# Performance work log

Hardware: AMD Instinct MI355X
Metric: run time of the kernel (lower is better)

The kernel has to match this reference:

```python
import jax, jax.numpy as jnp
import numpy as np

N_NODES = 200000
N_EDGES = 600000
N_GRAPHS = 10000
F_NODE = 32
F_EDGE = 16
H = 128
BN_EPS = 1e-5


def setup_inputs() -> dict:
    key = jax.random.key(0)
    ks = jax.random.split(key, 16)

    def rn(k, shape, scale=0.05):
        return jax.random.normal(k, shape, jnp.float32) * scale

    inp = {}
    inp['x'] = jax.random.normal(ks[0], (N_NODES, F_NODE), jnp.float32)
    inp['edge_index'] = jax.random.randint(ks[1], (2, N_EDGES), 0, N_NODES)
    inp['edge_attr'] = jax.random.normal(ks[2], (N_EDGES, F_EDGE), jnp.float32)
    inp['batch'] = jnp.sort(jax.random.randint(ks[3], (N_NODES,), 0, N_GRAPHS))
    # GIN MLP params for 3 conv layers: Linear(din,H) -> BN(H) -> ReLU -> Linear(H,H)
    dims = [F_NODE, H, H]
    i = 4
    for l, din in enumerate(dims, 1):
        inp[f'w1_{l}'] = rn(ks[i], (din, H)); i += 1
        inp[f'b1_{l}'] = jnp.zeros((H,), jnp.float32)
        inp[f'gamma_{l}'] = jnp.ones((H,), jnp.float32)
        inp[f'beta_{l}'] = jnp.zeros((H,), jnp.float32)
        inp[f'rmean_{l}'] = jnp.zeros((H,), jnp.float32)  # BN running stats (eval mode)
        inp[f'rvar_{l}'] = jnp.ones((H,), jnp.float32)
        inp[f'w2_{l}'] = rn(ks[i], (H, H)); i += 1
        inp[f'b2_{l}'] = jnp.zeros((H,), jnp.float32)
    inp['w_e'] = rn(ks[i], (F_EDGE, H)); i += 1
    inp['b_e'] = jnp.zeros((H,), jnp.float32)
    inp['w_fc1'] = rn(ks[i], (H, H // 2)); i += 1
    inp['b_fc1'] = jnp.zeros((H // 2,), jnp.float32)
    inp['w_fc2'] = rn(ks[i], (H // 2, 1)); i += 1
    inp['b_fc2'] = jnp.zeros((1,), jnp.float32)
    return inp


def _gin_conv(x, edge_index, w1, b1, gamma, beta, rmean, rvar, w2, b2):
    # GINConv with eps=0: mlp((1+eps)*x + sum_{j in N(i)} x_j)
    src, dst = edge_index[0], edge_index[1]
    agg = jax.ops.segment_sum(x[src], dst, num_segments=N_NODES)  # scatter-add
    h = x + agg
    h = h @ w1 + b1
    h = (h - rmean) * jax.lax.rsqrt(rvar + BN_EPS) * gamma + beta  # BN eval mode
    h = jax.nn.relu(h)
    return h @ w2 + b2


def reference(x, edge_index, edge_attr, batch,
              w1_1, b1_1, gamma_1, beta_1, rmean_1, rvar_1, w2_1, b2_1,
              w1_2, b1_2, gamma_2, beta_2, rmean_2, rvar_2, w2_2, b2_2,
              w1_3, b1_3, gamma_3, beta_3, rmean_3, rvar_3, w2_3, b2_3,
              w_e, b_e, w_fc1, b_fc1, w_fc2, b_fc2):
    # edge embedding is computed in the original forward but never used
    _edge_emb = edge_attr @ w_e + b_e
    h = jax.nn.relu(_gin_conv(x, edge_index, w1_1, b1_1, gamma_1, beta_1, rmean_1, rvar_1, w2_1, b2_1))
    h = jax.nn.relu(_gin_conv(h, edge_index, w1_2, b1_2, gamma_2, beta_2, rmean_2, rvar_2, w2_2, b2_2))
    h = jax.nn.relu(_gin_conv(h, edge_index, w1_3, b1_3, gamma_3, beta_3, rmean_3, rvar_3, w2_3, b2_3))
    pooled = jax.ops.segment_sum(h, batch, num_segments=N_GRAPHS)  # global_add_pool
    h = jax.nn.relu(pooled @ w_fc1 + b_fc1)
    # dropout: identity in eval mode
    return h @ w_fc2 + b_fc2  # [N_GRAPHS, 1]
```

## Files before the change

kernel.cpp:

```cpp
#include <hip/hip_runtime.h>

#define N_NODES 200000
#define N_EDGES 600000
#define N_GRAPHS 10000
#define F_NODE 32
#define HDIM 128
#define BN_EPS 1e-5f

typedef unsigned short ushort_t;
typedef unsigned int uint_t;
typedef __attribute__((ext_vector_type(8))) short short8;
typedef __attribute__((ext_vector_type(4))) float f32x4;

__device__ __forceinline__ ushort_t f2bf(float f) {
    uint_t u = __builtin_bit_cast(uint_t, f);
    u += 0x7FFFu + ((u >> 16) & 1u);
    return (ushort_t)(u >> 16);
}
__device__ __forceinline__ float bf2f(ushort_t h) {
    uint_t u = ((uint_t)h) << 16;
    return __builtin_bit_cast(float, u);
}

__global__ __launch_bounds__(256) void fill_zero_k(uint_t* __restrict__ p, long long n)
{
    long long gid = (long long)blockIdx.x * blockDim.x + threadIdx.x;
    long long stride = (long long)gridDim.x * blockDim.x;
    for (long long i = gid; i < n; i += stride) p[i] = 0u;
}

__global__ __launch_bounds__(256) void cvt_bf16_k(
    const float* __restrict__ in, ushort_t* __restrict__ outp, long long n8)
{
    long long gid = (long long)blockIdx.x * blockDim.x + threadIdx.x;
    if (gid >= n8) return;
    const float4* ip = (const float4*)(in + gid * 8);
    float4 a = ip[0], b = ip[1];
    uint4 u;
    u.x = (uint_t)f2bf(a.x) | ((uint_t)f2bf(a.y) << 16);
    u.y = (uint_t)f2bf(a.z) | ((uint_t)f2bf(a.w) << 16);
    u.z = (uint_t)f2bf(b.x) | ((uint_t)f2bf(b.y) << 16);
    u.w = (uint_t)f2bf(b.z) | ((uint_t)f2bf(b.w) << 16);
    *reinterpret_cast<uint4*>(outp + gid * 8) = u;
}

__global__ __launch_bounds__(256) void hist_k(const int* __restrict__ dst, int* __restrict__ deg)
{
    int e = blockIdx.x * 256 + threadIdx.x;
    if (e < N_EDGES) atomicAdd(&deg[dst[e]], 1);
}

__global__ __launch_bounds__(256) void scan_blocks_k(
    const int* __restrict__ deg, int* __restrict__ incl, int* __restrict__ bsum)
{
    __shared__ int sh[256];
    int i = blockIdx.x * 256 + threadIdx.x;
    int v = (i < N_NODES) ? deg[i] : 0;
    sh[threadIdx.x] = v;
    __syncthreads();
    #pragma unroll
    for (int off = 1; off < 256; off <<= 1) {
        int t = (threadIdx.x >= off) ? sh[threadIdx.x - off] : 0;
        __syncthreads();
        sh[threadIdx.x] += t;
        __syncthreads();
    }
    if (i < N_NODES) incl[i] = sh[threadIdx.x];
    if (threadIdx.x == 255) bsum[blockIdx.x] = sh[255];
}

__global__ __launch_bounds__(256) void scan_bsum_k(int* __restrict__ bsum, int nb)
{
    __shared__ int sh[256];
    int run = 0;
    for (int base = 0; base < nb; base += 256) {
        int i = base + threadIdx.x;
        int v = (i < nb) ? bsum[i] : 0;
        sh[threadIdx.x] = v;
        __syncthreads();
        #pragma unroll
        for (int off = 1; off < 256; off <<= 1) {
            int t = (threadIdx.x >= off) ? sh[threadIdx.x - off] : 0;
            __syncthreads();
            sh[threadIdx.x] += t;
            __syncthreads();
        }
        if (i < nb) bsum[i] = run + sh[threadIdx.x] - v;
        run += sh[255];
        __syncthreads();
    }
}

__global__ __launch_bounds__(256) void finalize_csr_k(
    const int* __restrict__ deg, const int* __restrict__ incl,
    const int* __restrict__ bsum, int* __restrict__ rowptr, int* __restrict__ cursor)
{
    int i = blockIdx.x * 256 + threadIdx.x;
    if (i >= N_NODES) return;
    int v = incl[i] + bsum[blockIdx.x];
    rowptr[i + 1] = v;
    cursor[i] = v - deg[i];
    if (i == 0) rowptr[0] = 0;
}

__global__ __launch_bounds__(256) void fill_edges_k(
    const int* __restrict__ src, const int* __restrict__ dst,
    int* __restrict__ cursor, int* __restrict__ col)
{
    int e = blockIdx.x * 256 + threadIdx.x;
    if (e >= N_EDGES) return;
    int pos = atomicAdd(&cursor[dst[e]], 1);
    col[pos] = src[e];
}

template<int K>
__global__ __launch_bounds__(256) void permute_w_k(
    const float* __restrict__ w, ushort_t* __restrict__ wp)
{
    constexpr int KS = K / 32;
    int gid = blockIdx.x * 256 + threadIdx.x;
    if (gid >= K * HDIM) return;
    int idx = gid;
    int j = idx & 7; idx >>= 3;
    int lane = idx & 63; idx >>= 6;
    int ks = idx % KS;
    int ntg = idx / KS;
    int k = ks * 32 + ((lane >> 4) << 3) + j;
    int n = ntg * 16 + (lane & 15);
    wp[gid] = f2bf(w[k * HDIM + n]);
}

template<int K, bool POOL>
__global__ __launch_bounds__(256) void fused_layer_k(
    const ushort_t* __restrict__ xin, const int* __restrict__ rowptr,
    const int* __restrict__ col, const ushort_t* __restrict__ wp1,
    const float* __restrict__ b1, const float* __restrict__ gamma,
    const float* __restrict__ beta, const float* __restrict__ rmean,
    const float* __restrict__ rvar, const ushort_t* __restrict__ wp2,
    const float* __restrict__ b2, ushort_t* __restrict__ out,
    const int* __restrict__ batch, float* __restrict__ pooled)
{
    constexpr int KS1 = K / 32;
    constexpr int KS2 = 4;
    constexpr int LDA = K + 8;
    constexpr int LDT = HDIM + 8;
    constexpr int FPT = K / 4;
    constexpr int NV  = FPT / 8;
    __shared__ ushort_t A_lds[64 * LDT];
    __shared__ int batch_l[64];

    const int tid  = threadIdx.x;
    const int lane = tid & 63;
    const int wid  = tid >> 6;
    const int wm   = wid >> 1;
    const int wn   = wid & 1;
    const long long m0 = (long long)blockIdx.x * 64;

    if (POOL && tid < 64) batch_l[tid] = batch[m0 + tid];

    {
        int row = tid >> 2;
        int fq  = (tid & 3) * FPT;
        long long n = m0 + row;
        float acc[FPT];
        {
            const uint4* xp = (const uint4*)(xin + n * (long long)K + fq);
            #pragma unroll
            for (int v = 0; v < NV; ++v) {
                uint4 u = xp[v];
                acc[v*8+0]=bf2f(u.x&0xffff); acc[v*8+1]=bf2f(u.x>>16);
                acc[v*8+2]=bf2f(u.y&0xffff); acc[v*8+3]=bf2f(u.y>>16);
                acc[v*8+4]=bf2f(u.z&0xffff); acc[v*8+5]=bf2f(u.z>>16);
                acc[v*8+6]=bf2f(u.w&0xffff); acc[v*8+7]=bf2f(u.w>>16);
            }
        }
        const int p0 = rowptr[n], p1 = rowptr[n + 1];
        int p = p0;
        for (; p + 2 <= p1; p += 2) {
            long long s0 = col[p];
            long long s1 = col[p + 1];
            const uint4* sp0 = (const uint4*)(xin + s0 * K + fq);
            const uint4* sp1 = (const uint4*)(xin + s1 * K + fq);
            uint4 u0[NV], u1[NV];
            #pragma unroll
            for (int v = 0; v < NV; ++v) u0[v] = sp0[v];
            #pragma unroll
            for (int v = 0; v < NV; ++v) u1[v] = sp1[v];
            #pragma unroll
            for (int v = 0; v < NV; ++v) {
                acc[v*8+0]+=bf2f(u0[v].x&0xffff)+bf2f(u1[v].x&0xffff);
                acc[v*8+1]+=bf2f(u0[v].x>>16)   +bf2f(u1[v].x>>16);
                acc[v*8+2]+=bf2f(u0[v].y&0xffff)+bf2f(u1[v].y&0xffff);
                acc[v*8+3]+=bf2f(u0[v].y>>16)   +bf2f(u1[v].y>>16);
                acc[v*8+4]+=bf2f(u0[v].z&0xffff)+bf2f(u1[v].z&0xffff);
                acc[v*8+5]+=bf2f(u0[v].z>>16)   +bf2f(u1[v].z>>16);
                acc[v*8+6]+=bf2f(u0[v].w&0xffff)+bf2f(u1[v].w&0xffff);
                acc[v*8+7]+=bf2f(u0[v].w>>16)   +bf2f(u1[v].w>>16);
            }
        }
        if (p < p1) {
            long long s = col[p];
            const uint4* sp = (const uint4*)(xin + s * K + fq);
            uint4 u[NV];
            #pragma unroll
            for (int v = 0; v < NV; ++v) u[v] = sp[v];
            #pragma unroll
            for (int v = 0; v < NV; ++v) {
                acc[v*8+0]+=bf2f(u[v].x&0xffff); acc[v*8+1]+=bf2f(u[v].x>>16);
                acc[v*8+2]+=bf2f(u[v].y&0xffff); acc[v*8+3]+=bf2f(u[v].y>>16);
                acc[v*8+4]+=bf2f(u[v].z&0xffff); acc[v*8+5]+=bf2f(u[v].z>>16);
                acc[v*8+6]+=bf2f(u[v].w&0xffff); acc[v*8+7]+=bf2f(u[v].w>>16);
            }
        }
        #pragma unroll
        for (int f = 0; f < FPT; f += 2) {
            uint_t pk = (uint_t)f2bf(acc[f]) | ((uint_t)f2bf(acc[f+1]) << 16);
            *reinterpret_cast<uint_t*>(&A_lds[row * LDA + fq + f]) = pk;
        }
    }
    __syncthreads();

    f32x4 acc1[2][4] = {};
    {
        short8 bfrag[4][KS1];
        #pragma unroll
        for (int nt = 0; nt < 4; ++nt)
            #pragma unroll
            for (int ks = 0; ks < KS1; ++ks) {
                int ntg = wn * 4 + nt;
                bfrag[nt][ks] = *reinterpret_cast<const short8*>(
                    wp1 + ((((ntg * KS1) + ks) * 64 + lane) << 3));
            }
        #pragma unroll
        for (int ks = 0; ks < KS1; ++ks) {
            short8 afrag[2];
            #pragma unroll
            for (int mt = 0; mt < 2; ++mt) {
                int row = wm * 32 + mt * 16 + (lane & 15);
                int c   = ks * 32 + ((lane >> 4) << 3);
                afrag[mt] = *reinterpret_cast<const short8*>(&A_lds[row * LDA + c]);
            }
            #pragma unroll
            for (int mt = 0; mt < 2; ++mt)
                #pragma unroll
                for (int nt = 0; nt < 4; ++nt)
                    acc1[mt][nt] = __builtin_amdgcn_mfma_f32_16x16x32_bf16(
                        afrag[mt], bfrag[nt][ks], acc1[mt][nt], 0, 0, 0);
        }
    }
    __syncthreads();

    #pragma unroll
    for (int nt = 0; nt < 4; ++nt) {
        int c = wn * 64 + nt * 16 + (lane & 15);
        float rs = rsqrtf(rvar[c] + BN_EPS);
        float scale = gamma[c] * rs;
        float shift = (b1[c] - rmean[c]) * scale + beta[c];
        #pragma unroll
        for (int mt = 0; mt < 2; ++mt) {
            int rowb = wm * 32 + mt * 16 + ((lane >> 4) << 2);
            #pragma unroll
            for (int r = 0; r < 4; ++r) {
                float v = fmaxf(acc1[mt][nt][r] * scale + shift, 0.f);
                A_lds[(rowb + r) * LDT + c] = f2bf(v);
            }
        }
    }
    __syncthreads();

    f32x4 acc2[2][4] = {};
    {
        short8 bfrag[4][KS2];
        #pragma unroll
        for (int nt = 0; nt < 4; ++nt)
            #pragma unroll
            for (int ks = 0; ks < KS2; ++ks) {
                int ntg = wn * 4 + nt;
                bfrag[nt][ks] = *reinterpret_cast<const short8*>(
                    wp2 + ((((ntg * KS2) + ks) * 64 + lane) << 3));
            }
        #pragma unroll
        for (int ks = 0; ks < KS2; ++ks) {
            short8 afrag[2];
            #pragma unroll
            for (int mt = 0; mt < 2; ++mt) {
                int row = wm * 32 + mt * 16 + (lane & 15);
                int c   = ks * 32 + ((lane >> 4) << 3);
                afrag[mt] = *reinterpret_cast<const short8*>(&A_lds[row * LDT + c]);
            }
            #pragma unroll
            for (int mt = 0; mt < 2; ++mt)
                #pragma unroll
                for (int nt = 0; nt < 4; ++nt)
                    acc2[mt][nt] = __builtin_amdgcn_mfma_f32_16x16x32_bf16(
                        afrag[mt], bfrag[nt][ks], acc2[mt][nt], 0, 0, 0);
        }
    }

    if (!POOL) {
        #pragma unroll
        for (int nt = 0; nt < 4; ++nt) {
            int c = wn * 64 + nt * 16 + (lane & 15);
            float bias = b2[c];
            #pragma unroll
            for (int mt = 0; mt < 2; ++mt) {
                long long rowb = m0 + wm * 32 + mt * 16 + ((lane >> 4) << 2);
                #pragma unroll
                for (int r = 0; r < 4; ++r) {
                    float v = fmaxf(acc2[mt][nt][r] + bias, 0.f);
                    out[(rowb + r) * HDIM + c] = f2bf(v);
                }
            }
        }
    } else {
        __syncthreads();
        #pragma unroll
        for (int nt = 0; nt < 4; ++nt) {
            int c = wn * 64 + nt * 16 + (lane & 15);
            float bias = b2[c];
            #pragma unroll
            for (int mt = 0; mt < 2; ++mt) {
                int rowb = wm * 32 + mt * 16 + ((lane >> 4) << 2);
                #pragma unroll
                for (int r = 0; r < 4; ++r) {
                    float v = fmaxf(acc2[mt][nt][r] + bias, 0.f);
                    A_lds[(rowb + r) * LDT + c] = f2bf(v);
                }
            }
        }
        __syncthreads();
        if (tid < HDIM) {
            int colw = tid;
            int curb = batch_l[0];
            float s = 0.f;
            #pragma unroll 8
            for (int r = 0; r < 64; ++r) {
                int b = batch_l[r];
                if (b != curb) {
                    atomicAdd(&pooled[(long long)curb * HDIM + colw], s);
                    curb = b; s = 0.f;
                }
                s += bf2f(A_lds[r * LDT + colw]);
            }
            atomicAdd(&pooled[(long long)curb * HDIM + colw], s);
        }
    }
}

__global__ __launch_bounds__(64) void fc_head_k(
    const float* __restrict__ pooled,
    const float* __restrict__ w_fc1, const float* __restrict__ b_fc1,
    const float* __restrict__ w_fc2, const float* __restrict__ b_fc2,
    float* __restrict__ out)
{
    int g = blockIdx.x;
    int j = threadIdx.x;
    __shared__ float p[HDIM];
    p[j]      = pooled[(long long)g * HDIM + j];
    p[j + 64] = pooled[(long long)g * HDIM + j + 64];
    __syncthreads();

    float acc = b_fc1[j];
    #pragma unroll 8
    for (int k = 0; k < HDIM; ++k) acc += p[k] * w_fc1[k * 64 + j];
    acc = fmaxf(acc, 0.f);

    float v = acc * w_fc2[j];
    #pragma unroll
    for (int off = 32; off > 0; off >>= 1) v += __shfl_down(v, off, 64);
    if (j == 0) out[g] = v + b_fc2[0];
}

extern "C" void kernel_launch(void* const* d_in, const int* in_sizes, int n_in,
                              void* d_out, int out_size, void* d_ws, size_t ws_size,
                              hipStream_t stream) {
    const float* x     = (const float*)d_in[0];
    const int*   ei    = (const int*)d_in[1];
    const int*   src   = ei;
    const int*   dst   = ei + N_EDGES;
    const int*   batch = (const int*)d_in[3];
    const float* L[3][8];
    for (int l = 0; l < 3; ++l)
        for (int p = 0; p < 8; ++p)
            L[l][p] = (const float*)d_in[4 + 8 * l + p];
    const float* w_fc1 = (const float*)d_in[30];
    const float* b_fc1 = (const float*)d_in[31];
    const float* w_fc2 = (const float*)d_in[32];
    const float* b_fc2 = (const float*)d_in[33];
    float* out = (float*)d_out;

    char* base = (char*)d_ws;
    ushort_t* hA     = (ushort_t*)(base);
    ushort_t* hB     = (ushort_t*)(base + 51200000);
    ushort_t* xbf    = (ushort_t*)(base + 102400000);
    float*    pooled = (float*)   (base + 115200000);
    ushort_t* wpBase = (ushort_t*)(base + 120320000);
    int*      deg    = (int*)     (base + 120800000);
    int*      incl   = (int*)     (base + 121600000);
    int*      bsum   = (int*)     (base + 122400000);
    int*      rowptr = (int*)     (base + 122404096);
    int*      cursor = (int*)     (base + 123204100);
    int*      colarr = (int*)     (base + 124004100);

    ushort_t* wp1_1 = wpBase;
    ushort_t* wp2_1 = wp1_1 + 32 * HDIM;
    ushort_t* wp1_2 = wp2_1 + HDIM * HDIM;
    ushort_t* wp2_2 = wp1_2 + HDIM * HDIM;
    ushort_t* wp1_3 = wp2_2 + HDIM * HDIM;
    ushort_t* wp2_3 = wp1_3 + HDIM * HDIM;

    const int GEMM_GRID = N_NODES / 64;
    const int NB_NODE   = (N_NODES + 255) / 256;
    const int NB_EDGE   = (N_EDGES + 255) / 256;

    permute_w_k<F_NODE><<<(F_NODE * HDIM + 255) / 256, 256, 0, stream>>>(L[0][0], wp1_1);
    permute_w_k<HDIM><<<(HDIM * HDIM + 255) / 256, 256, 0, stream>>>(L[0][6], wp2_1);
    permute_w_k<HDIM><<<(HDIM * HDIM + 255) / 256, 256, 0, stream>>>(L[1][0], wp1_2);
    permute_w_k<HDIM><<<(HDIM * HDIM + 255) / 256, 256, 0, stream>>>(L[1][6], wp2_2);
    permute_w_k<HDIM><<<(HDIM * HDIM + 255) / 256, 256, 0, stream>>>(L[2][0], wp1_3);
    permute_w_k<HDIM><<<(HDIM * HDIM + 255) / 256, 256, 0, stream>>>(L[2][6], wp2_3);
    {
        long long n8 = (long long)N_NODES * F_NODE / 8;
        cvt_bf16_k<<<(int)((n8 + 255) / 256), 256, 0, stream>>>(x, xbf, n8);
    }

    fill_zero_k<<<512, 256, 0, stream>>>((uint_t*)deg, N_NODES);
    hist_k<<<NB_EDGE, 256, 0, stream>>>(dst, deg);
    scan_blocks_k<<<NB_NODE, 256, 0, stream>>>(deg, incl, bsum);
    scan_bsum_k<<<1, 256, 0, stream>>>(bsum, NB_NODE);
    finalize_csr_k<<<NB_NODE, 256, 0, stream>>>(deg, incl, bsum, rowptr, cursor);
    fill_edges_k<<<NB_EDGE, 256, 0, stream>>>(src, dst, cursor, colarr);

    fill_zero_k<<<512, 256, 0, stream>>>((uint_t*)pooled, (long long)N_GRAPHS * HDIM);

    fused_layer_k<F_NODE, false><<<GEMM_GRID, 256, 0, stream>>>(
        xbf, rowptr, colarr, wp1_1, L[0][1], L[0][2], L[0][3], L[0][4], L[0][5],
        wp2_1, L[0][7], hA, nullptr, nullptr);
    fused_layer_k<HDIM, false><<<GEMM_GRID, 256, 0, stream>>>(
        hA, rowptr, colarr, wp1_2, L[1][1], L[1][2], L[1][3], L[1][4], L[1][5],
        wp2_2, L[1][7], hB, nullptr, nullptr);
    fused_layer_k<HDIM, true><<<GEMM_GRID, 256, 0, stream>>>(
        hB, rowptr, colarr, wp1_3, L[2][1], L[2][2], L[2][3], L[2][4], L[2][5],
        wp2_3, L[2][7], nullptr, batch, pooled);

    fc_head_k<<<N_GRAPHS, 64, 0, stream>>>(pooled, w_fc1, b_fc1, w_fc2, b_fc2, out);
}
```

Baseline: 264.2 us.

## Split neighbor gather across edges per thread and merge prep launches

The aggregation in each fused layer now splits a node's neighbor list across the threads of a row group (edge-parallel) as well as across feature slices, and combines the partial sums with xor shuffles. Each thread then gathers wider feature chunks (layer 1 full 32 features, layers 2/3 half rows), which cuts per-neighbor serial latency and raises memory-level parallelism. The six weight-permute launches and the input conversion are merged into one prep kernel, and the two zero-fills into one by relocating deg right after pooled. The costs are more registers per thread for larger accumulators, extra shuffle reductions, and branchy per-thread LDS writes.

```diff
diff --git a/kernel.cpp b/kernel.cpp
--- a/kernel.cpp
+++ b/kernel.cpp
@@ -29,19 +29,43 @@
     for (long long i = gid; i < n; i += stride) p[i] = 0u;
 }
 
-__global__ __launch_bounds__(256) void cvt_bf16_k(
-    const float* __restrict__ in, ushort_t* __restrict__ outp, long long n8)
-{
-    long long gid = (long long)blockIdx.x * blockDim.x + threadIdx.x;
-    if (gid >= n8) return;
-    const float4* ip = (const float4*)(in + gid * 8);
-    float4 a = ip[0], b = ip[1];
-    uint4 u;
-    u.x = (uint_t)f2bf(a.x) | ((uint_t)f2bf(a.y) << 16);
-    u.y = (uint_t)f2bf(a.z) | ((uint_t)f2bf(a.w) << 16);
-    u.z = (uint_t)f2bf(b.x) | ((uint_t)f2bf(b.y) << 16);
-    u.w = (uint_t)f2bf(b.z) | ((uint_t)f2bf(b.w) << 16);
-    *reinterpret_cast<uint4*>(outp + gid * 8) = u;
+__global__ __launch_bounds__(256) void prep_k(
+    const float* __restrict__ w1_1, const float* __restrict__ w2_1,
+    const float* __restrict__ w1_2, const float* __restrict__ w2_2,
+    const float* __restrict__ w1_3, const float* __restrict__ w2_3,
+    ushort_t* __restrict__ wp, const float* __restrict__ x, ushort_t* __restrict__ xbf)
+{
+    int gid = blockIdx.x * 256 + threadIdx.x;
+    if (gid < 86016) {
+        const float* w; int lidx; int K;
+        if (gid < 4096)       { w = w1_1; lidx = gid;         K = 32; }
+        else if (gid < 20480) { w = w2_1; lidx = gid - 4096;  K = 128; }
+        else if (gid < 36864) { w = w1_2; lidx = gid - 20480; K = 128; }
+        else if (gid < 53248) { w = w2_2; lidx = gid - 36864; K = 128; }
+        else if (gid < 69632) { w = w1_3; lidx = gid - 53248; K = 128; }
+        else                  { w = w2_3; lidx = gid - 69632; K = 128; }
+        int KS = K / 32;
+        int idx = lidx;
+        int j = idx & 7; idx >>= 3;
+        int lane = idx & 63; idx >>= 6;
+        int ks = idx % KS;
+        int ntg = idx / KS;
+        int k = ks * 32 + ((lane >> 4) << 3) + j;
+        int n = ntg * 16 + (lane & 15);
+        wp[gid] = f2bf(w[k * HDIM + n]);
+    } else {
+        long long i8 = gid - 86016;
+        if (i8 < (long long)N_NODES * F_NODE / 8) {
+            const float4* ip = (const float4*)(x + i8 * 8);
+            float4 a = ip[0], b = ip[1];
+            uint4 u;
+            u.x = (uint_t)f2bf(a.x) | ((uint_t)f2bf(a.y) << 16);
+            u.y = (uint_t)f2bf(a.z) | ((uint_t)f2bf(a.w) << 16);
+            u.z = (uint_t)f2bf(b.x) | ((uint_t)f2bf(b.y) << 16);
+            u.w = (uint_t)f2bf(b.z) | ((uint_t)f2bf(b.w) << 16);
+            *reinterpret_cast<uint4*>(xbf + i8 * 8) = u;
+        }
+    }
 }
 
 __global__ __launch_bounds__(256) void hist_k(const int* __restrict__ dst, int* __restrict__ deg)
@@ -113,24 +137,7 @@
     col[pos] = src[e];
 }
 
-template<int K>
-__global__ __launch_bounds__(256) void permute_w_k(
-    const float* __restrict__ w, ushort_t* __restrict__ wp)
-{
-    constexpr int KS = K / 32;
-    int gid = blockIdx.x * 256 + threadIdx.x;
-    if (gid >= K * HDIM) return;
-    int idx = gid;
-    int j = idx & 7; idx >>= 3;
-    int lane = idx & 63; idx >>= 6;
-    int ks = idx % KS;
-    int ntg = idx / KS;
-    int k = ks * 32 + ((lane >> 4) << 3) + j;
-    int n = ntg * 16 + (lane & 15);
-    wp[gid] = f2bf(w[k * HDIM + n]);
-}
-
-template<int K, bool POOL>
+template<int K, int FS, int ES, bool POOL>
 __global__ __launch_bounds__(256) void fused_layer_k(
     const ushort_t* __restrict__ xin, const int* __restrict__ rowptr,
     const int* __restrict__ col, const ushort_t* __restrict__ wp1,
@@ -144,8 +151,9 @@
     constexpr int KS2 = 4;
     constexpr int LDA = K + 8;
     constexpr int LDT = HDIM + 8;
-    constexpr int FPT = K / 4;
+    constexpr int FPT = K / FS;
     constexpr int NV  = FPT / 8;
+    constexpr int CH  = FPT / ES;
     __shared__ ushort_t A_lds[64 * LDT];
     __shared__ int batch_l[64];
 
@@ -159,11 +167,14 @@
     if (POOL && tid < 64) batch_l[tid] = batch[m0 + tid];
 
     {
-        int row = tid >> 2;
-        int fq  = (tid & 3) * FPT;
+        const int row = tid >> 2;
+        const int sub = tid & 3;
+        const int fh  = sub / ES;
+        const int eh  = sub % ES;
+        const int fq  = fh * FPT;
         long long n = m0 + row;
         float acc[FPT];
-        {
+        if (eh == 0) {
             const uint4* xp = (const uint4*)(xin + n * (long long)K + fq);
             #pragma unroll
             for (int v = 0; v < NV; ++v) {
@@ -173,34 +184,14 @@
                 acc[v*8+4]=bf2f(u.z&0xffff); acc[v*8+5]=bf2f(u.z>>16);
                 acc[v*8+6]=bf2f(u.w&0xffff); acc[v*8+7]=bf2f(u.w>>16);
             }
+        } else {
+            #pragma unroll
+            for (int f = 0; f < FPT; ++f) acc[f] = 0.f;
         }
         const int p0 = rowptr[n], p1 = rowptr[n + 1];
-        int p = p0;
-        for (; p + 2 <= p1; p += 2) {
-            long long s0 = col[p];
-            long long s1 = col[p + 1];
-            const uint4* sp0 = (const uint4*)(xin + s0 * K + fq);
-            const uint4* sp1 = (const uint4*)(xin + s1 * K + fq);
-            uint4 u0[NV], u1[NV];
-            #pragma unroll
-            for (int v = 0; v < NV; ++v) u0[v] = sp0[v];
-            #pragma unroll
-            for (int v = 0; v < NV; ++v) u1[v] = sp1[v];
-            #pragma unroll
-            for (int v = 0; v < NV; ++v) {
-                acc[v*8+0]+=bf2f(u0[v].x&0xffff)+bf2f(u1[v].x&0xffff);
-                acc[v*8+1]+=bf2f(u0[v].x>>16)   +bf2f(u1[v].x>>16);
-                acc[v*8+2]+=bf2f(u0[v].y&0xffff)+bf2f(u1[v].y&0xffff);
-                acc[v*8+3]+=bf2f(u0[v].y>>16)   +bf2f(u1[v].y>>16);
-                acc[v*8+4]+=bf2f(u0[v].z&0xffff)+bf2f(u1[v].z&0xffff);
-                acc[v*8+5]+=bf2f(u0[v].z>>16)   +bf2f(u1[v].z>>16);
-                acc[v*8+6]+=bf2f(u0[v].w&0xffff)+bf2f(u1[v].w&0xffff);
-                acc[v*8+7]+=bf2f(u0[v].w>>16)   +bf2f(u1[v].w>>16);
-            }
-        }
-        if (p < p1) {
+        for (int p = p0 + eh; p < p1; p += ES) {
             long long s = col[p];
-            const uint4* sp = (const uint4*)(xin + s * K + fq);
+            const uint4* sp = (const uint4*)(xin + s * (long long)K + fq);
             uint4 u[NV];
             #pragma unroll
             for (int v = 0; v < NV; ++v) u[v] = sp[v];
@@ -213,9 +204,21 @@
             }
         }
         #pragma unroll
-        for (int f = 0; f < FPT; f += 2) {
-            uint_t pk = (uint_t)f2bf(acc[f]) | ((uint_t)f2bf(acc[f+1]) << 16);
-            *reinterpret_cast<uint_t*>(&A_lds[row * LDA + fq + f]) = pk;
+        for (int m = 1; m < ES; m <<= 1) {
+            #pragma unroll
+            for (int f = 0; f < FPT; ++f)
+                acc[f] += __shfl_xor(acc[f], m, 64);
+        }
+        #pragma unroll
+        for (int ee = 0; ee < ES; ++ee) {
+            if (eh == ee) {
+                #pragma unroll
+                for (int f = 0; f < CH; f += 2) {
+                    uint_t pk = (uint_t)f2bf(acc[ee*CH + f]) |
+                                ((uint_t)f2bf(acc[ee*CH + f + 1]) << 16);
+                    *reinterpret_cast<uint_t*>(&A_lds[row * LDA + fq + ee*CH + f]) = pk;
+                }
+            }
         }
     }
     __syncthreads();
@@ -394,52 +397,47 @@
     ushort_t* hB     = (ushort_t*)(base + 51200000);
     ushort_t* xbf    = (ushort_t*)(base + 102400000);
     float*    pooled = (float*)   (base + 115200000);
-    ushort_t* wpBase = (ushort_t*)(base + 120320000);
-    int*      deg    = (int*)     (base + 120800000);
-    int*      incl   = (int*)     (base + 121600000);
-    int*      bsum   = (int*)     (base + 122400000);
-    int*      rowptr = (int*)     (base + 122404096);
-    int*      cursor = (int*)     (base + 123204100);
-    int*      colarr = (int*)     (base + 124004100);
-
-    ushort_t* wp1_1 = wpBase;
-    ushort_t* wp2_1 = wp1_1 + 32 * HDIM;
-    ushort_t* wp1_2 = wp2_1 + HDIM * HDIM;
-    ushort_t* wp2_2 = wp1_2 + HDIM * HDIM;
-    ushort_t* wp1_3 = wp2_2 + HDIM * HDIM;
-    ushort_t* wp2_3 = wp1_3 + HDIM * HDIM;
+    int*      deg    = (int*)     (base + 120320000);
+    int*      incl   = (int*)     (base + 121120000);
+    int*      bsum   = (int*)     (base + 121920000);
+    int*      rowptr = (int*)     (base + 121924096);
+    int*      cursor = (int*)     (base + 122724112);
+    int*      colarr = (int*)     (base + 123524112);
+    ushort_t* wp     = (ushort_t*)(base + 125924112);
+
+    ushort_t* wp1_1 = wp;
+    ushort_t* wp2_1 = wp + 4096;
+    ushort_t* wp1_2 = wp + 20480;
+    ushort_t* wp2_2 = wp + 36864;
+    ushort_t* wp1_3 = wp + 53248;
+    ushort_t* wp2_3 = wp + 69632;
 
     const int GEMM_GRID = N_NODES / 64;
     const int NB_NODE   = (N_NODES + 255) / 256;
     const int NB_EDGE   = (N_EDGES + 255) / 256;
 
-    permute_w_k<F_NODE><<<(F_NODE * HDIM + 255) / 256, 256, 0, stream>>>(L[0][0], wp1_1);
-    permute_w_k<HDIM><<<(HDIM * HDIM + 255) / 256, 256, 0, stream>>>(L[0][6], wp2_1);
-    permute_w_k<HDIM><<<(HDIM * HDIM + 255) / 256, 256, 0, stream>>>(L[1][0], wp1_2);
-    permute_w_k<HDIM><<<(HDIM * HDIM + 255) / 256, 256, 0, stream>>>(L[1][6], wp2_2);
-    permute_w_k<HDIM><<<(HDIM * HDIM + 255) / 256, 256, 0, stream>>>(L[2][0], wp1_3);
-    permute_w_k<HDIM><<<(HDIM * HDIM + 255) / 256, 256, 0, stream>>>(L[2][6], wp2_3);
+    fill_zero_k<<<512, 256, 0, stream>>>((uint_t*)pooled,
+        (long long)N_GRAPHS * HDIM + N_NODES);
+
     {
-        long long n8 = (long long)N_NODES * F_NODE / 8;
-        cvt_bf16_k<<<(int)((n8 + 255) / 256), 256, 0, stream>>>(x, xbf, n8);
-    }
-
-    fill_zero_k<<<512, 256, 0, stream>>>((uint_t*)deg, N_NODES);
+        long long tot = 86016 + (long long)N_NODES * F_NODE / 8;
+        prep_k<<<(int)((tot + 255) / 256), 256, 0, stream>>>(
+            L[0][0], L[0][6], L[1][0], L[1][6], L[2][0], L[2][6], wp, x, xbf);
+    }
+
     hist_k<<<NB_EDGE, 256, 0, stream>>>(dst, deg);
     scan_blocks_k<<<NB_NODE, 256, 0, stream>>>(deg, incl, bsum);
     scan_bsum_k<<<1, 256, 0, stream>>>(bsum, NB_NODE);
     finalize_csr_k<<<NB_NODE, 256, 0, stream>>>(deg, incl, bsum, rowptr, cursor);
     fill_edges_k<<<NB_EDGE, 256, 0, stream>>>(src, dst, cursor, colarr);
 
-    fill_zero_k<<<512, 256, 0, stream>>>((uint_t*)pooled, (long long)N_GRAPHS * HDIM);
-
-    fused_layer_k<F_NODE, false><<<GEMM_GRID, 256, 0, stream>>>(
+    fused_layer_k<F_NODE, 1, 4, false><<<GEMM_GRID, 256, 0, stream>>>(
         xbf, rowptr, colarr, wp1_1, L[0][1], L[0][2], L[0][3], L[0][4], L[0][5],
         wp2_1, L[0][7], hA, nullptr, nullptr);
-    fused_layer_k<HDIM, false><<<GEMM_GRID, 256, 0, stream>>>(
+    fused_layer_k<HDIM, 2, 2, false><<<GEMM_GRID, 256, 0, stream>>>(
         hA, rowptr, colarr, wp1_2, L[1][1], L[1][2], L[1][3], L[1][4], L[1][5],
         wp2_2, L[1][7], hB, nullptr, nullptr);
-    fused_layer_k<HDIM, true><<<GEMM_GRID, 256, 0, stream>>>(
+    fused_layer_k<HDIM, 2, 2, true><<<GEMM_GRID, 256, 0, stream>>>(
         hB, rowptr, colarr, wp1_3, L[2][1], L[2][2], L[2][3], L[2][4], L[2][5],
         wp2_3, L[2][7], nullptr, batch, pooled);
 
```

Result: slower. 302.4 us (+14.5%).
